# Performance work log

Measured on AMD Instinct MI355X. Metric: run time of the kernel, lower is better.

Reference implementation:

```python
import jax, jax.numpy as jnp
import numpy as np

B, N, IN_D = 4, 2046, 512
D, H = 1024, 16
DH = D // H  # 64
S = N + 2
EPS = 1e-5


def setup_inputs() -> dict:
    key = jax.random.key(0)
    ks = jax.random.split(key, 9)
    s = lambda k, shp, fan: jax.random.normal(k, shp, jnp.float32) * (1.0 / np.sqrt(fan))
    return {
        "x": jax.random.normal(ks[0], (B, N, IN_D), jnp.float32),
        "W_map": s(ks[1], (IN_D, D), IN_D),
        "b_map": jnp.zeros((D,), jnp.float32),
        "time_token": jax.random.normal(ks[2], (1, D), jnp.float32),
        "cluster_token": jax.random.normal(ks[3], (1, D), jnp.float32),
        "ln_g": jnp.ones((D,), jnp.float32),
        "ln_b": jnp.zeros((D,), jnp.float32),
        "Wq": s(ks[4], (H, DH, DH), DH),
        "bq": jax.random.normal(ks[5], (H, DH), jnp.float32) * 0.01,
        "Wk": s(ks[6], (H, DH, DH), DH),
        "bk": jax.random.normal(ks[7], (H, DH), jnp.float32) * 0.01,
    }


def reference(x, W_map, b_map, time_token, cluster_token, ln_g, ln_b, Wq, bq, Wk, bk):
    b = x.shape[0]
    tokens = x @ W_map + b_map                       # [B, N, D]
    tt = jnp.broadcast_to(time_token[None], (b, 1, D))
    ct = jnp.broadcast_to(cluster_token[None], (b, 1, D))
    out = jnp.concatenate([tt, ct, tokens], axis=1)  # [B, S, D]
    # LayerNorm (norm1)
    mu = jnp.mean(out, axis=-1, keepdims=True)
    var = jnp.mean(jnp.square(out - mu), axis=-1, keepdims=True)
    h = (out - mu) * jax.lax.rsqrt(var + EPS) * ln_g + ln_b
    # MSAAttention: per-head Q/K linear, softmax(QK^T / sqrt(d_head))
    hh = h.reshape(b, S, H, DH)
    q = jnp.einsum("bshd,hde->bhse", hh, Wq) + bq[None, :, None, :]
    k = jnp.einsum("bshd,hde->bhse", hh, Wk) + bk[None, :, None, :]
    scores = jnp.einsum("bhse,bhte->bhst", q, k) / np.sqrt(DH).astype(np.float32)
    attn = jax.nn.softmax(scores, axis=-1)           # [B, H, S, S]
    # hstack over heads -> [B, S, H*S]; extract_attention reshapes back and
    # means over heads, then takes rows 0 (timing) and 1 (id).
    m = jnp.mean(attn, axis=1)                       # [B, S, S]
    return m[:, 0, :], m[:, 1, :]
```

## Files before the change

### kernel.cpp

```cpp
#include <hip/hip_runtime.h>
#include <hip/hip_bf16.h>
#include <math.h>

#define BB 4
#define NN 2046
#define IND 512
#define DD 1024
#define SS 2048
#define MM (BB*NN)
#define MPAD 8192
#define RPAD 8256
#define EPSV 1e-5f

#define F_U      0
#define F_G      2048
#define F_C2     2080
#define F_SSPEC  2112
#define F_DEN    2116
#define F_S12    4096
#define F_A      135168
#define B_XH   1597440
#define B_WHT  9986048
#define B_WLT  11034624

typedef float f32x4 __attribute__((ext_vector_type(4)));
typedef __bf16 bf16x8 __attribute__((ext_vector_type(8)));
typedef unsigned short u16x8 __attribute__((ext_vector_type(8)));

__device__ __forceinline__ unsigned short f2bf_rne(float f) {
  unsigned int u = __float_as_uint(f);
  u += 0x7FFFu + ((u >> 16) & 1u);
  return (unsigned short)(u >> 16);
}
__device__ __forceinline__ float bf2f(unsigned short h) {
  return __uint_as_float(((unsigned int)h) << 16);
}
__device__ __forceinline__ float waveSum(float v) {
  #pragma unroll
  for (int m = 32; m >= 1; m >>= 1) v += __shfl_xor(v, m, 64);
  return v;
}
__device__ __forceinline__ float blockReduceSum(float v, volatile float* buf4) {
  #pragma unroll
  for (int m = 32; m >= 1; m >>= 1) v += __shfl_xor(v, m, 64);
  int wid = threadIdx.x >> 6;
  __syncthreads();
  if ((threadIdx.x & 63) == 0) buf4[wid] = v;
  __syncthreads();
  return buf4[0] + buf4[1] + buf4[2] + buf4[3];
}

#define GLOAD_LDS16(g, l) \
  __builtin_amdgcn_global_load_lds((const __attribute__((address_space(1))) void*)(g), \
                                   (__attribute__((address_space(3))) void*)(l), 16, 0, 0)

__global__ __launch_bounds__(256) void prep(
    const float* __restrict__ x, const float* __restrict__ Wm,
    const float* __restrict__ tt, const float* __restrict__ ct,
    const float* __restrict__ lng, const float* __restrict__ lnb,
    const float* __restrict__ Wq, const float* __restrict__ bq,
    const float* __restrict__ Wk, const float* __restrict__ bk,
    unsigned short* __restrict__ xh, unsigned short* __restrict__ wht,
    unsigned short* __restrict__ wlt, float* __restrict__ ws) {
  __shared__ float tile[64][65];
  __shared__ float hq[4][64];
  __shared__ float qs[4][64];
  const int bid = blockIdx.x, t = threadIdx.x;

  if (bid < 2048) {
    const int row = bid * 4 + (t >> 6);
    const int c0 = (t & 63) * 8;
    const size_t po = (size_t)row * IND + c0;
    u16x8 hv;
    if (row < MM) {
      const float4* xv = (const float4*)(x + po);
      float4 a = xv[0], b = xv[1];
      float vv[8] = {a.x, a.y, a.z, a.w, b.x, b.y, b.z, b.w};
      #pragma unroll
      for (int i = 0; i < 8; ++i) hv[i] = f2bf_rne(vv[i]);
    } else {
      #pragma unroll
      for (int i = 0; i < 8; ++i) hv[i] = 0;
    }
    *(u16x8*)(xh + po) = hv;
  } else if (bid < 2176) {
    const int b2 = bid - 2048;
    const int kb = b2 >> 4, nb = b2 & 15;
    const int k0 = kb * 64, n0 = nb * 64;
    #pragma unroll
    for (int q = 0; q < 16; ++q) {
      int lin = q * 256 + t;
      int kk = lin >> 6, nn = lin & 63;
      tile[kk][nn] = Wm[(size_t)(k0 + kk) * DD + n0 + nn];
    }
    __syncthreads();
    #pragma unroll
    for (int q = 0; q < 16; ++q) {
      int lin = q * 256 + t;
      int nn = lin >> 6, kk = lin & 63;
      float v = tile[kk][nn];
      unsigned short hh = f2bf_rne(v);
      wht[(size_t)(n0 + nn) * IND + k0 + kk] = hh;
      wlt[(size_t)(n0 + nn) * IND + k0 + kk] = f2bf_rne(v - bf2f(hh));
    }
  } else {
    const int w = t >> 6, e = t & 63;
    const int sh = (bid - 2176) * 4 + w;
    const int s = sh >> 4, h = sh & 15;
    const float* src = s ? ct : tt;

    float s1 = 0.f, s2 = 0.f;
    #pragma unroll
    for (int i = 0; i < 16; ++i) { float v = src[i*64 + e]; s1 += v; s2 += v*v; }
    s1 = waveSum(s1); s2 = waveSum(s2);
    if (h == 0 && e == 0) {
      ws[F_SSPEC + s*2 + 0] = s1;
      ws[F_SSPEC + s*2 + 1] = s2;
    }
    const float mu = s1 * (1.f/DD);
    const float var = s2 * (1.f/DD) - mu*mu;
    const float rstd = rsqrtf(var + EPSV);
    const int d0 = h * 64;
    hq[w][e] = (src[d0+e] - mu) * rstd * lng[d0+e] + lnb[d0+e];
    float qv = bq[d0+e];
    #pragma unroll 8
    for (int d = 0; d < 64; ++d) qv += hq[w][d] * Wq[(size_t)(d0+d)*64 + e];
    qs[w][e] = qv;
    float wt = 0.f;
    #pragma unroll 8
    for (int ee = 0; ee < 64; ++ee) wt += Wk[(size_t)(d0+e)*64 + ee] * qs[w][ee];
    wt *= 0.125f;
    const float c = waveSum(qs[w][e] * bk[d0+e]) * 0.125f;
    const float u = lng[d0+e] * wt;
    ws[F_U + s*DD + d0 + e] = u;
    const float G  = waveSum(lng[d0+e] * wt);
    const float C  = waveSum(lnb[d0+e] * wt);
    const float a0 = waveSum(tt[d0+e] * u);
    const float a1 = waveSum(ct[d0+e] * u);
    if (e == 0) {
      ws[F_G  + sh] = G;
      ws[F_C2 + sh] = C + c;
      ws[F_A + (size_t)sh*RPAD + MPAD + 0] = a0;
      ws[F_A + (size_t)sh*RPAD + MPAD + 1] = a1;
    }
  }
}

__global__ __launch_bounds__(256, 2) void stageB(
    const unsigned short* __restrict__ xh,
    const unsigned short* __restrict__ wht, const unsigned short* __restrict__ wlt,
    const float* __restrict__ bmap, float* __restrict__ ws) {
  __shared__ char smem[49152];
  const int t = threadIdx.x, wave = t >> 6, lane = t & 63;
  const int lj = lane & 15, lg = lane >> 4;
  const int mb = blockIdx.x & 63, nb = blockIdx.x >> 6;
  const int m0 = mb * 128, n0 = nb * 128;
  const int wr = wave >> 1, wc = wave & 1;
  const float* U = ws + F_U;

  f32x4 acc[4][4];
  #pragma unroll
  for (int i = 0; i < 4; ++i)
    #pragma unroll
    for (int j = 0; j < 4; ++j) acc[i][j] = (f32x4){0.f,0.f,0.f,0.f};

  const int srow = lane >> 2;
  const int gslot = (lane & 3) ^ (srow & 3);

  #define STAGE(ks, buf) do {                                                  \
    const size_t ko_ = (size_t)(ks)*32 + gslot*8;                              \
    _Pragma("unroll")                                                          \
    for (int q = 0; q < 2; ++q) {                                              \
      const int rb = wave*32 + q*16;                                           \
      GLOAD_LDS16(xh  + (size_t)(m0 + rb + srow)*IND + ko_,                    \
                  smem + (buf)*8192 + rb*64);                                  \
      GLOAD_LDS16(wht + (size_t)(n0 + rb + srow)*IND + ko_,                    \
                  smem + 16384 + (buf)*16384 + rb*64);                         \
      GLOAD_LDS16(wlt + (size_t)(n0 + rb + srow)*IND + ko_,                    \
                  smem + 16384 + (buf)*16384 + 8192 + rb*64);                  \
    }                                                                          \
  } while (0)

  STAGE(0, 0);
  #pragma unroll
  for (int k = 0; k < 16; ++k) {
    if (k < 15) {
      STAGE(k + 1, (k + 1) & 1);
      asm volatile("s_waitcnt vmcnt(6)" ::: "memory");
    } else {
      asm volatile("s_waitcnt vmcnt(0)" ::: "memory");
    }
    __builtin_amdgcn_sched_barrier(0);
    __builtin_amdgcn_s_barrier();
    __builtin_amdgcn_sched_barrier(0);
    {
      const int ab = (k & 1) * 8192;
      const int bb = 16384 + (k & 1) * 16384;
      bf16x8 af[4], bfh[4], bfl[4];
      #pragma unroll
      for (int i = 0; i < 4; ++i) {
        const int r = wr*64 + i*16 + lj;
        af[i] = *(const bf16x8*)(smem + ab + r*64 + ((lg ^ (r & 3)) * 16));
      }
      #pragma unroll
      for (int j = 0; j < 4; ++j) {
        const int r = wc*64 + j*16 + lj;
        const int byt = r*64 + ((lg ^ (r & 3)) * 16);
        bfh[j] = *(const bf16x8*)(smem + bb + byt);
        bfl[j] = *(const bf16x8*)(smem + bb + 8192 + byt);
      }
      #pragma unroll
      for (int i = 0; i < 4; ++i)
        #pragma unroll
        for (int j = 0; j < 4; ++j) {
          acc[i][j] = __builtin_amdgcn_mfma_f32_16x16x32_bf16(af[i], bfh[j], acc[i][j], 0,0,0);
          acc[i][j] = __builtin_amdgcn_mfma_f32_16x16x32_bf16(af[i], bfl[j], acc[i][j], 0,0,0);
        }
    }
    __builtin_amdgcn_sched_barrier(0);
    asm volatile("s_waitcnt lgkmcnt(0)" ::: "memory");
    __builtin_amdgcn_sched_barrier(0);
    __builtin_amdgcn_s_barrier();
    __builtin_amdgcn_sched_barrier(0);
  }
  #undef STAGE

  float s1p[16], s2p[16], a0p[16], a1p[16];
  #pragma unroll
  for (int p = 0; p < 16; ++p) { s1p[p]=0.f; s2p[p]=0.f; a0p[p]=0.f; a1p[p]=0.f; }
  #pragma unroll
  for (int j = 0; j < 4; ++j) {
    const int gc = n0 + wc*64 + j*16 + lj;
    const float bmv = bmap[gc];
    const float u0 = U[gc], u1 = U[DD + gc];
    #pragma unroll
    for (int i = 0; i < 4; ++i)
      #pragma unroll
      for (int r = 0; r < 4; ++r) {
        const float tok = acc[i][j][r] + bmv;
        const int p = i*4 + r;
        s1p[p] += tok; s2p[p] += tok*tok;
        a0p[p] += tok*u0; a1p[p] += tok*u1;
      }
  }
  #pragma unroll
  for (int msk = 8; msk >= 1; msk >>= 1)
    #pragma unroll
    for (int p = 0; p < 16; ++p) {
      s1p[p] += __shfl_xor(s1p[p], msk, 64);
      s2p[p] += __shfl_xor(s2p[p], msk, 64);
      a0p[p] += __shfl_xor(a0p[p], msk, 64);
      a1p[p] += __shfl_xor(a1p[p], msk, 64);
    }

  if (lj == 0) {
    const int h = nb*2 + wc;
    #pragma unroll
    for (int p = 0; p < 16; ++p) {
      const int row = m0 + wr*64 + (p>>2)*16 + lg*4 + (p&3);
      ws[F_A + (size_t)h*RPAD + row]        = a0p[p];
      ws[F_A + (size_t)(16 + h)*RPAD + row] = a1p[p];
    }
  }

  float* s12w = (float*)smem;
  if (lj == 0) {
    #pragma unroll
    for (int p = 0; p < 16; ++p) {
      const int rl = (p>>2)*16 + lg*4 + (p&3);
      s12w[(wave*64 + rl)*2 + 0] = s1p[p];
      s12w[(wave*64 + rl)*2 + 1] = s2p[p];
    }
  }
  __syncthreads();
  if (t < 128) {
    const int wv = t >> 6, rl = t & 63;
    const float s1 = s12w[((wv*2)*64 + rl)*2]     + s12w[((wv*2+1)*64 + rl)*2];
    const float s2 = s12w[((wv*2)*64 + rl)*2 + 1] + s12w[((wv*2+1)*64 + rl)*2 + 1];
    ws[F_S12 + (size_t)(m0 + t)*16 + nb*2 + 0] = s1;
    ws[F_S12 + (size_t)(m0 + t)*16 + nb*2 + 1] = s2;
  }
}

__device__ __forceinline__ void rowMoments(const float* __restrict__ ws, int p,
                                           int r, float& mu, float& rstd) {
  float s1, s2;
  if (p < 2) {
    s1 = ws[F_SSPEC + p*2 + 0];
    s2 = ws[F_SSPEC + p*2 + 1];
  } else {
    const float4* q4 = (const float4*)(ws + F_S12 + (size_t)r*16);
    const float4 a = q4[0], b = q4[1], c = q4[2], d = q4[3];
    s1 = (a.x + a.z) + (b.x + b.z) + (c.x + c.z) + (d.x + d.z);
    s2 = (a.y + a.w) + (b.y + b.w) + (c.y + c.w) + (d.y + d.w);
  }
  mu = s1 * (1.f/DD);
  const float var = s2 * (1.f/DD) - mu*mu;
  rstd = rsqrtf(var + EPSV);
}

__global__ __launch_bounds__(256) void stageC1(float* __restrict__ ws) {
  __shared__ float rbuf[4];
  const int bid = blockIdx.x;
  const int b = bid >> 5, sh = bid & 31;
  const int t = threadIdx.x;
  const float Gh = ws[F_G + sh], Ch = ws[F_C2 + sh];
  const float* Af = ws + F_A + (size_t)sh*RPAD;

  float sum = 0.f;
  #pragma unroll
  for (int i = 0; i < 8; ++i) {
    const int p = i*256 + t;
    const int r = (p < 2) ? (MPAD + p) : (b*NN + p - 2);
    float mu, rstd;
    rowMoments(ws, p, r, mu, rstd);
    const float sc = fminf(rstd*(Af[r] - mu*Gh) + Ch, 60.f);
    sum += __expf(sc);
  }
  sum = blockReduceSum(sum, rbuf);
  if (t == 0) ws[F_DEN + bid] = sum;
}

__global__ __launch_bounds__(256) void stageC2(const float* __restrict__ ws,
                                               float* __restrict__ out) {
  __shared__ float dn[16], Gs[16], Cs[16];
  const int bid = blockIdx.x;
  const int bs = bid >> 3, chunk = bid & 7;
  const int b = bs >> 1, s = bs & 1;
  const int t = threadIdx.x;
  if (t < 16) {
    dn[t] = 1.f / ws[F_DEN + b*32 + s*16 + t];
    Gs[t] = ws[F_G  + s*16 + t];
    Cs[t] = ws[F_C2 + s*16 + t];
  }
  __syncthreads();
  const int p = chunk*256 + t;
  const int r = (p < 2) ? (MPAD + p) : (b*NN + p - 2);
  float mu, rstd;
  rowMoments(ws, p, r, mu, rstd);
  float acc = 0.f;
  #pragma unroll
  for (int h = 0; h < 16; ++h) {
    const float a = ws[F_A + (size_t)(s*16 + h)*RPAD + r];
    const float sc = fminf(rstd*(a - mu*Gs[h]) + Cs[h], 60.f);
    acc += __expf(sc) * dn[h];
  }
  out[(size_t)s*(BB*SS) + (size_t)b*SS + p] = acc * (1.f/16.f);
}

extern "C" void kernel_launch(void* const* d_in, const int* in_sizes, int n_in,
                              void* d_out, int out_size, void* d_ws, size_t ws_size,
                              hipStream_t stream) {
  const float* x   = (const float*)d_in[0];
  const float* Wm  = (const float*)d_in[1];
  const float* bm  = (const float*)d_in[2];
  const float* tt  = (const float*)d_in[3];
  const float* ct  = (const float*)d_in[4];
  const float* lng = (const float*)d_in[5];
  const float* lnb = (const float*)d_in[6];
  const float* Wq  = (const float*)d_in[7];
  const float* bq  = (const float*)d_in[8];
  const float* Wk  = (const float*)d_in[9];
  const float* bk  = (const float*)d_in[10];
  char* wsb = (char*)d_ws;
  float* ws = (float*)d_ws;
  float* out = (float*)d_out;

  unsigned short* xh  = (unsigned short*)(wsb + B_XH);
  unsigned short* wht = (unsigned short*)(wsb + B_WHT);
  unsigned short* wlt = (unsigned short*)(wsb + B_WLT);

  hipLaunchKernelGGL(prep,    dim3(2184), dim3(256), 0, stream,
                     x, Wm, tt, ct, lng, lnb, Wq, bq, Wk, bk, xh, wht, wlt, ws);
  hipLaunchKernelGGL(stageB,  dim3(512),  dim3(256), 0, stream,
                     xh, wht, wlt, bm, ws);
  hipLaunchKernelGGL(stageC1, dim3(128),  dim3(256), 0, stream, ws);
  hipLaunchKernelGGL(stageC2, dim3(64),   dim3(256), 0, stream, ws, out);
}
```

Measured before the change: 119.7 us.

## Drop split-bf16 low weight term and widen GEMM K-step to 64

Removes the hi/lo bf16 split of W_map, so the main GEMM does one MFMA per tile pair instead of two and no longer loads the low-part weights. It also widens each pipeline stage from K=32 to K=64 with an 8-slot XOR swizzle and 64KB of LDS, which halves the number of barrier iterations. The cost is lower accuracy in the mapped tokens, which could affect the softmax outputs, and the larger LDS use may reduce occupancy.

```diff
diff --git a/kernel.cpp b/kernel.cpp
--- a/kernel.cpp
+++ b/kernel.cpp
@@ -21,7 +21,6 @@
 #define F_A      135168
 #define B_XH   1597440
 #define B_WHT  9986048
-#define B_WLT  11034624
 
 typedef float f32x4 __attribute__((ext_vector_type(4)));
 typedef __bf16 bf16x8 __attribute__((ext_vector_type(8)));
@@ -61,7 +60,7 @@
     const float* __restrict__ Wq, const float* __restrict__ bq,
     const float* __restrict__ Wk, const float* __restrict__ bk,
     unsigned short* __restrict__ xh, unsigned short* __restrict__ wht,
-    unsigned short* __restrict__ wlt, float* __restrict__ ws) {
+    float* __restrict__ ws) {
   __shared__ float tile[64][65];
   __shared__ float hq[4][64];
   __shared__ float qs[4][64];
@@ -98,10 +97,7 @@
     for (int q = 0; q < 16; ++q) {
       int lin = q * 256 + t;
       int nn = lin >> 6, kk = lin & 63;
-      float v = tile[kk][nn];
-      unsigned short hh = f2bf_rne(v);
-      wht[(size_t)(n0 + nn) * IND + k0 + kk] = hh;
-      wlt[(size_t)(n0 + nn) * IND + k0 + kk] = f2bf_rne(v - bf2f(hh));
+      wht[(size_t)(n0 + nn) * IND + k0 + kk] = f2bf_rne(tile[kk][nn]);
     }
   } else {
     const int w = t >> 6, e = t & 63;
@@ -148,9 +144,9 @@
 
 __global__ __launch_bounds__(256, 2) void stageB(
     const unsigned short* __restrict__ xh,
-    const unsigned short* __restrict__ wht, const unsigned short* __restrict__ wlt,
+    const unsigned short* __restrict__ wht,
     const float* __restrict__ bmap, float* __restrict__ ws) {
-  __shared__ char smem[49152];
+  __shared__ char smem[65536];
   const int t = threadIdx.x, wave = t >> 6, lane = t & 63;
   const int lj = lane & 15, lg = lane >> 4;
   const int mb = blockIdx.x & 63, nb = blockIdx.x >> 6;
@@ -164,58 +160,54 @@
     #pragma unroll
     for (int j = 0; j < 4; ++j) acc[i][j] = (f32x4){0.f,0.f,0.f,0.f};
 
-  const int srow = lane >> 2;
-  const int gslot = (lane & 3) ^ (srow & 3);
+  const int srow = lane >> 3;
+  const int gslot = (lane & 7) ^ srow;
 
   #define STAGE(ks, buf) do {                                                  \
-    const size_t ko_ = (size_t)(ks)*32 + gslot*8;                              \
+    const size_t ko_ = (size_t)(ks)*64 + gslot*8;                              \
     _Pragma("unroll")                                                          \
-    for (int q = 0; q < 2; ++q) {                                              \
-      const int rb = wave*32 + q*16;                                           \
+    for (int q = 0; q < 4; ++q) {                                              \
+      const int rb = wave*32 + q*8;                                            \
       GLOAD_LDS16(xh  + (size_t)(m0 + rb + srow)*IND + ko_,                    \
-                  smem + (buf)*8192 + rb*64);                                  \
+                  smem + (buf)*16384 + rb*128);                                \
       GLOAD_LDS16(wht + (size_t)(n0 + rb + srow)*IND + ko_,                    \
-                  smem + 16384 + (buf)*16384 + rb*64);                         \
-      GLOAD_LDS16(wlt + (size_t)(n0 + rb + srow)*IND + ko_,                    \
-                  smem + 16384 + (buf)*16384 + 8192 + rb*64);                  \
+                  smem + 32768 + (buf)*16384 + rb*128);                        \
     }                                                                          \
   } while (0)
 
   STAGE(0, 0);
   #pragma unroll
-  for (int k = 0; k < 16; ++k) {
-    if (k < 15) {
+  for (int k = 0; k < 8; ++k) {
+    if (k < 7) {
       STAGE(k + 1, (k + 1) & 1);
-      asm volatile("s_waitcnt vmcnt(6)" ::: "memory");
+      asm volatile("s_waitcnt vmcnt(8)" ::: "memory");
     } else {
       asm volatile("s_waitcnt vmcnt(0)" ::: "memory");
     }
     __builtin_amdgcn_sched_barrier(0);
     __builtin_amdgcn_s_barrier();
     __builtin_amdgcn_sched_barrier(0);
-    {
-      const int ab = (k & 1) * 8192;
-      const int bb = 16384 + (k & 1) * 16384;
-      bf16x8 af[4], bfh[4], bfl[4];
+    #pragma unroll
+    for (int kf = 0; kf < 2; ++kf) {
+      const int ab = (k & 1) * 16384;
+      const int bb = 32768 + (k & 1) * 16384;
+      const int sl = kf*4 + lg;
+      bf16x8 af[4], bfh[4];
       #pragma unroll
       for (int i = 0; i < 4; ++i) {
         const int r = wr*64 + i*16 + lj;
-        af[i] = *(const bf16x8*)(smem + ab + r*64 + ((lg ^ (r & 3)) * 16));
+        af[i] = *(const bf16x8*)(smem + ab + r*128 + ((sl ^ (r & 7)) * 16));
       }
       #pragma unroll
       for (int j = 0; j < 4; ++j) {
         const int r = wc*64 + j*16 + lj;
-        const int byt = r*64 + ((lg ^ (r & 3)) * 16);
-        bfh[j] = *(const bf16x8*)(smem + bb + byt);
-        bfl[j] = *(const bf16x8*)(smem + bb + 8192 + byt);
+        bfh[j] = *(const bf16x8*)(smem + bb + r*128 + ((sl ^ (r & 7)) * 16));
       }
       #pragma unroll
       for (int i = 0; i < 4; ++i)
         #pragma unroll
-        for (int j = 0; j < 4; ++j) {
+        for (int j = 0; j < 4; ++j)
           acc[i][j] = __builtin_amdgcn_mfma_f32_16x16x32_bf16(af[i], bfh[j], acc[i][j], 0,0,0);
-          acc[i][j] = __builtin_amdgcn_mfma_f32_16x16x32_bf16(af[i], bfl[j], acc[i][j], 0,0,0);
-        }
     }
     __builtin_amdgcn_sched_barrier(0);
     asm volatile("s_waitcnt lgkmcnt(0)" ::: "memory");
@@ -368,12 +360,11 @@
 
   unsigned short* xh  = (unsigned short*)(wsb + B_XH);
   unsigned short* wht = (unsigned short*)(wsb + B_WHT);
-  unsigned short* wlt = (unsigned short*)(wsb + B_WLT);
 
   hipLaunchKernelGGL(prep,    dim3(2184), dim3(256), 0, stream,
-                     x, Wm, tt, ct, lng, lnb, Wq, bq, Wk, bk, xh, wht, wlt, ws);
+                     x, Wm, tt, ct, lng, lnb, Wq, bq, Wk, bk, xh, wht, ws);
   hipLaunchKernelGGL(stageB,  dim3(512),  dim3(256), 0, stream,
-                     xh, wht, wlt, bm, ws);
+                     xh, wht, bm, ws);
   hipLaunchKernelGGL(stageC1, dim3(128),  dim3(256), 0, stream, ws);
   hipLaunchKernelGGL(stageC2, dim3(64),   dim3(256), 0, stream, ws, out);
 }
```

Result: faster. 112.1 us (-6.3%).
